# Kernel tuning notes

Measured on AMD Instinct MI355X. Metric: run time of the kernel, lower is better.

## Reference

```python
import jax, jax.numpy as jnp
import numpy as np

B, S, D, H = 1, 4096, 1024, 16
DH = D // H

def setup_inputs() -> dict:
    key = jax.random.key(0)
    ks = jax.random.split(key, 5)
    std = float(np.sqrt(2.0 / (D + D)))
    return {
        "x": jax.random.normal(ks[0], (B, S, D), dtype=jnp.float32),
        "Wq": jax.random.normal(ks[1], (D, D), dtype=jnp.float32) * std,
        "Wk": jax.random.normal(ks[2], (D, D), dtype=jnp.float32) * std,
        "Wv": jax.random.normal(ks[3], (D, D), dtype=jnp.float32) * std,
        "Wo": jax.random.normal(ks[4], (D, D), dtype=jnp.float32) * std,
    }

def reference(x, Wq, Wk, Wv, Wo):
    # projections: input @ W.T, then split heads: b s (h d) -> b h s d
    def split_heads(t):
        b, s, _ = t.shape
        return t.reshape(b, s, H, DH).transpose(0, 2, 1, 3)
    q = split_heads(x @ Wq.T)
    k = split_heads(x @ Wk.T)
    v = split_heads(x @ Wv.T)
    scale = 1.0 / jnp.sqrt(jnp.asarray(DH, dtype=x.dtype))
    scores = jnp.einsum("bhqd,bhkd->bhqk", q, k) * scale  # (b,h,s,s)
    # causal mask: allow k <= q
    causal = jnp.tril(jnp.ones((S, S), dtype=bool))
    scores = jnp.where(causal, scores, jnp.finfo(scores.dtype).min)
    attn = jax.nn.softmax(scores, axis=-1)
    out = jnp.einsum("bhqk,bhkd->bhqd", attn, v)  # (b,h,s,d)
    out = out.transpose(0, 2, 1, 3).reshape(B, S, D)  # b h s d -> b s (h d)
    return out @ Wo.T
```

## Files before the change

### kernel.cpp

```cpp
#include <hip/hip_runtime.h>
#include <math.h>

#define SEQ 4096
#define DM  1024
#define NH  16
#define DH  64

typedef _Float16 h16;
typedef __attribute__((ext_vector_type(4))) _Float16 h16x4;
typedef __attribute__((ext_vector_type(8))) _Float16 h16x8;
typedef __attribute__((ext_vector_type(4))) float f32x4;

__device__ __forceinline__ void gload_lds16(const h16* g, h16* l) {
    __builtin_amdgcn_global_load_lds(
        (const __attribute__((address_space(1))) void*)g,
        (__attribute__((address_space(3))) void*)l, 16, 0, 0);
}

__global__ __launch_bounds__(256) void cvt_f32_f16(const float* __restrict__ in,
                                                   h16* __restrict__ out, int n4) {
    const int i = blockIdx.x * 256 + threadIdx.x;
    if (i < n4) {
        const float4 v = ((const float4*)in)[i];
        h16x4 o = { (h16)v.x, (h16)v.y, (h16)v.z, (h16)v.w };
        ((h16x4*)out)[i] = o;
    }
}

#define GT 32

__global__ __launch_bounds__(256) void gemm_qkv(const h16* __restrict__ xh,
                                                const h16* __restrict__ Wq,
                                                const h16* __restrict__ Wk,
                                                const h16* __restrict__ Wv,
                                                h16* __restrict__ Qh,
                                                h16* __restrict__ Kh,
                                                h16* __restrict__ Vth,
                                                float scl) {
    __shared__ h16 As[128 * GT];
    __shared__ h16 Bs[128 * GT];

    const int z    = blockIdx.z;
    const h16* B   = (z == 0) ? Wq : (z == 1) ? Wk : Wv;
    const int t    = threadIdx.x;
    const int lane = t & 63;
    const int w    = t >> 6;
    const int wm   = (w >> 1) * 64;
    const int wn   = (w & 1) * 64;
    const int l15  = lane & 15;
    const int lq   = lane >> 4;
    const int lq8  = lq * 8;
    const int m0   = blockIdx.y * 128;
    const int n0   = blockIdx.x * 128;
    const int K = DM, M = SEQ, N = DM;

    const int srow = w * 16 + (lane >> 2);
    const int scol = (lane & 3) * 8;
    const h16* pa0 = xh + (size_t)(m0 + srow) * K + scol;
    const h16* pa1 = xh + (size_t)(m0 + 64 + srow) * K + scol;
    const h16* pb0 = B  + (size_t)(n0 + srow) * K + scol;
    const h16* pb1 = B  + (size_t)(n0 + 64 + srow) * K + scol;
    h16* const la0 = &As[w * 512];
    h16* const la1 = &As[2048 + w * 512];
    h16* const lb0 = &Bs[w * 512];
    h16* const lb1 = &Bs[2048 + w * 512];

    f32x4 acc[4][4] = {};

    for (int k0 = 0; k0 < K; k0 += 32) {
        __syncthreads();
        gload_lds16(pa0 + k0, la0);
        gload_lds16(pa1 + k0, la1);
        gload_lds16(pb0 + k0, lb0);
        gload_lds16(pb1 + k0, lb1);
        __syncthreads();

        h16x8 af[4], bf[4];
        #pragma unroll
        for (int i = 0; i < 4; ++i)
            af[i] = *(const h16x8*)&As[(wm + i * 16 + l15) * GT + lq8];
        #pragma unroll
        for (int j = 0; j < 4; ++j)
            bf[j] = *(const h16x8*)&Bs[(wn + j * 16 + l15) * GT + lq8];
        #pragma unroll
        for (int i = 0; i < 4; ++i)
            #pragma unroll
            for (int j = 0; j < 4; ++j)
                acc[i][j] = __builtin_amdgcn_mfma_f32_16x16x32_f16(af[i], bf[j], acc[i][j], 0, 0, 0);
    }

    const int cr = wm + lq * 4;
    const int cc = wn + l15;
    if (z == 2) {
        #pragma unroll
        for (int i = 0; i < 4; ++i)
            #pragma unroll
            for (int j = 0; j < 4; ++j) {
                const int gm0 = m0 + cr + i * 16;
                const int gn  = n0 + cc + j * 16;
                h16x4 v = { (h16)acc[i][j][0], (h16)acc[i][j][1],
                            (h16)acc[i][j][2], (h16)acc[i][j][3] };
                *(h16x4*)(Vth + (size_t)gn * M + gm0) = v;
            }
    } else {
        h16* Og = (z == 0) ? Qh : Kh;
        const float e = (z == 0) ? scl : 1.0f;
        #pragma unroll
        for (int i = 0; i < 4; ++i)
            #pragma unroll
            for (int j = 0; j < 4; ++j)
                #pragma unroll
                for (int r = 0; r < 4; ++r) {
                    const int gm = m0 + cr + i * 16 + r;
                    const int gn = n0 + cc + j * 16;
                    Og[(size_t)gm * N + gn] = (h16)(acc[i][j][r] * e);
                }
    }
}

__global__ __launch_bounds__(256) void gemm_out(const h16* __restrict__ A,
                                                const h16* __restrict__ B,
                                                float* __restrict__ C) {
    __shared__ h16 As[128 * GT];
    __shared__ h16 Bs[128 * GT];

    const int t    = threadIdx.x;
    const int lane = t & 63;
    const int w    = t >> 6;
    const int wm   = (w >> 1) * 64;
    const int wn   = (w & 1) * 64;
    const int l15  = lane & 15;
    const int lq   = lane >> 4;
    const int lq8  = lq * 8;
    const int m0   = blockIdx.y * 128;
    const int n0   = blockIdx.x * 128;
    const int K = DM, N = DM;

    const int srow = w * 16 + (lane >> 2);
    const int scol = (lane & 3) * 8;
    const h16* pa0 = A + (size_t)(m0 + srow) * K + scol;
    const h16* pa1 = A + (size_t)(m0 + 64 + srow) * K + scol;
    const h16* pb0 = B + (size_t)(n0 + srow) * K + scol;
    const h16* pb1 = B + (size_t)(n0 + 64 + srow) * K + scol;
    h16* const la0 = &As[w * 512];
    h16* const la1 = &As[2048 + w * 512];
    h16* const lb0 = &Bs[w * 512];
    h16* const lb1 = &Bs[2048 + w * 512];

    f32x4 acc[4][4] = {};

    for (int k0 = 0; k0 < K; k0 += 32) {
        __syncthreads();
        gload_lds16(pa0 + k0, la0);
        gload_lds16(pa1 + k0, la1);
        gload_lds16(pb0 + k0, lb0);
        gload_lds16(pb1 + k0, lb1);
        __syncthreads();

        h16x8 af[4], bf[4];
        #pragma unroll
        for (int i = 0; i < 4; ++i)
            af[i] = *(const h16x8*)&As[(wm + i * 16 + l15) * GT + lq8];
        #pragma unroll
        for (int j = 0; j < 4; ++j)
            bf[j] = *(const h16x8*)&Bs[(wn + j * 16 + l15) * GT + lq8];
        #pragma unroll
        for (int i = 0; i < 4; ++i)
            #pragma unroll
            for (int j = 0; j < 4; ++j)
                acc[i][j] = __builtin_amdgcn_mfma_f32_16x16x32_f16(af[i], bf[j], acc[i][j], 0, 0, 0);
    }

    const int cr = wm + lq * 4;
    const int cc = wn + l15;
    #pragma unroll
    for (int i = 0; i < 4; ++i)
        #pragma unroll
        for (int j = 0; j < 4; ++j)
            #pragma unroll
            for (int r = 0; r < 4; ++r)
                C[(size_t)(m0 + cr + i * 16 + r) * N + n0 + cc + j * 16] = acc[i][j][r];
}

#define AST 80

__device__ __forceinline__ void tile_softmax(f32x4 s[4], float& m_st, float& l_st,
                                             f32x4 o[4], h16* ps_row, bool diag,
                                             int q_loc, int lq) {
    if (diag) {
        #pragma unroll
        for (int jj = 0; jj < 4; ++jj)
            #pragma unroll
            for (int r = 0; r < 4; ++r)
                if ((jj * 16 + lq * 4 + r) > q_loc) s[jj][r] = -1e30f;
    }
    float mx = m_st;
    #pragma unroll
    for (int jj = 0; jj < 4; ++jj)
        #pragma unroll
        for (int r = 0; r < 4; ++r)
            mx = fmaxf(mx, s[jj][r]);
    mx = fmaxf(mx, __shfl_xor(mx, 16, 64));
    mx = fmaxf(mx, __shfl_xor(mx, 32, 64));
    const float alpha = exp2f(m_st - mx);
    m_st = mx;
    float sum = 0.0f;
    #pragma unroll
    for (int jj = 0; jj < 4; ++jj) {
        const float p0 = exp2f(s[jj][0] - mx);
        const float p1 = exp2f(s[jj][1] - mx);
        const float p2 = exp2f(s[jj][2] - mx);
        const float p3 = exp2f(s[jj][3] - mx);
        sum += (p0 + p1) + (p2 + p3);
        h16x4 pk = { (h16)p0, (h16)p1, (h16)p2, (h16)p3 };
        *(h16x4*)(ps_row + jj * 16 + lq * 4) = pk;
    }
    sum += __shfl_xor(sum, 16, 64);
    sum += __shfl_xor(sum, 32, 64);
    l_st = l_st * alpha + sum;
    #pragma unroll
    for (int jj = 0; jj < 4; ++jj)
        #pragma unroll
        for (int r = 0; r < 4; ++r)
            o[jj][r] *= alpha;
}

__global__ __launch_bounds__(256, 3) void flash_attn_mfma(
        const h16* __restrict__ Qg, const h16* __restrict__ Kg,
        const h16* __restrict__ Vt, h16* __restrict__ Og) {
    __shared__ h16 Ks[64 * AST];
    __shared__ h16 Vs[64 * AST];
    __shared__ h16 Ps[2][64 * AST];

    const int qA   = blockIdx.x;
    const int qB   = 63 - qA;
    const int hh   = blockIdx.y;
    const int t    = threadIdx.x;
    const int lane = t & 63;
    const int w    = t >> 6;
    const int l15  = lane & 15;
    const int lq   = lane >> 4;
    const int lq8  = lq * 8;
    const int hc   = hh * DH;
    const int q_loc = w * 16 + l15;

    const int r1 = t >> 3;
    const int r2 = r1 + 32;
    const int c1 = (t & 7) * 8;

    {
        const int qa0 = qA * 64, qb0 = qB * 64;
        *(h16x8*)&Ks[r1 * AST + c1] = *(const h16x8*)(Qg + (size_t)(qa0 + r1) * DM + hc + c1);
        *(h16x8*)&Ks[r2 * AST + c1] = *(const h16x8*)(Qg + (size_t)(qa0 + r2) * DM + hc + c1);
        *(h16x8*)&Vs[r1 * AST + c1] = *(const h16x8*)(Qg + (size_t)(qb0 + r1) * DM + hc + c1);
        *(h16x8*)&Vs[r2 * AST + c1] = *(const h16x8*)(Qg + (size_t)(qb0 + r2) * DM + hc + c1);
    }
    h16x8 kv1 = *(const h16x8*)(Kg + (size_t)(r1) * DM + hc + c1);
    h16x8 kv2 = *(const h16x8*)(Kg + (size_t)(r2) * DM + hc + c1);
    h16x8 vv1 = *(const h16x8*)(Vt + (size_t)(hc + r1) * SEQ + c1);
    h16x8 vv2 = *(const h16x8*)(Vt + (size_t)(hc + r2) * SEQ + c1);

    __syncthreads();
    h16x8 qfA[2], qfB[2];
    qfA[0] = *(const h16x8*)&Ks[q_loc * AST + lq8];
    qfA[1] = *(const h16x8*)&Ks[q_loc * AST + 32 + lq8];
    qfB[0] = *(const h16x8*)&Vs[q_loc * AST + lq8];
    qfB[1] = *(const h16x8*)&Vs[q_loc * AST + 32 + lq8];

    float mA = -1e30f, lA = 0.0f, mB = -1e30f, lB = 0.0f;
    f32x4 oA[4] = {}, oB[4] = {};
    h16* const psA = &Ps[0][(size_t)q_loc * AST];
    h16* const psB = &Ps[1][(size_t)q_loc * AST];

    int kt = 0;
    for (; kt <= qA; ++kt) {
        __syncthreads();
        *(h16x8*)&Ks[r1 * AST + c1] = kv1;
        *(h16x8*)&Ks[r2 * AST + c1] = kv2;
        *(h16x8*)&Vs[r1 * AST + c1] = vv1;
        *(h16x8*)&Vs[r2 * AST + c1] = vv2;
        __syncthreads();
        {
            const int k0n = (kt + 1) * 64;
            kv1 = *(const h16x8*)(Kg + (size_t)(k0n + r1) * DM + hc + c1);
            kv2 = *(const h16x8*)(Kg + (size_t)(k0n + r2) * DM + hc + c1);
            vv1 = *(const h16x8*)(Vt + (size_t)(hc + r1) * SEQ + k0n + c1);
            vv2 = *(const h16x8*)(Vt + (size_t)(hc + r2) * SEQ + k0n + c1);
        }

        f32x4 sA[4] = {}, sB[4] = {};
        #pragma unroll
        for (int kc = 0; kc < 2; ++kc)
            #pragma unroll
            for (int jj = 0; jj < 4; ++jj) {
                const h16x8 kf = *(const h16x8*)&Ks[(jj * 16 + l15) * AST + kc * 32 + lq8];
                sA[jj] = __builtin_amdgcn_mfma_f32_16x16x32_f16(kf, qfA[kc], sA[jj], 0, 0, 0);
                sB[jj] = __builtin_amdgcn_mfma_f32_16x16x32_f16(kf, qfB[kc], sB[jj], 0, 0, 0);
            }

        tile_softmax(sA, mA, lA, oA, psA, kt == qA, q_loc, lq);
        tile_softmax(sB, mB, lB, oB, psB, false, q_loc, lq);

        asm volatile("s_waitcnt lgkmcnt(0)" ::: "memory");
        h16x8 pfA[2], pfB[2];
        pfA[0] = *(const h16x8*)(psA + lq8);
        pfA[1] = *(const h16x8*)(psA + 32 + lq8);
        pfB[0] = *(const h16x8*)(psB + lq8);
        pfB[1] = *(const h16x8*)(psB + 32 + lq8);

        #pragma unroll
        for (int kc = 0; kc < 2; ++kc)
            #pragma unroll
            for (int jj = 0; jj < 4; ++jj) {
                const h16x8 vf = *(const h16x8*)&Vs[(jj * 16 + l15) * AST + kc * 32 + lq8];
                oA[jj] = __builtin_amdgcn_mfma_f32_16x16x32_f16(vf, pfA[kc], oA[jj], 0, 0, 0);
                oB[jj] = __builtin_amdgcn_mfma_f32_16x16x32_f16(vf, pfB[kc], oB[jj], 0, 0, 0);
            }
    }
    for (; kt <= qB; ++kt) {
        __syncthreads();
        *(h16x8*)&Ks[r1 * AST + c1] = kv1;
        *(h16x8*)&Ks[r2 * AST + c1] = kv2;
        *(h16x8*)&Vs[r1 * AST + c1] = vv1;
        *(h16x8*)&Vs[r2 * AST + c1] = vv2;
        __syncthreads();
        if (kt < qB) {
            const int k0n = (kt + 1) * 64;
            kv1 = *(const h16x8*)(Kg + (size_t)(k0n + r1) * DM + hc + c1);
            kv2 = *(const h16x8*)(Kg + (size_t)(k0n + r2) * DM + hc + c1);
            vv1 = *(const h16x8*)(Vt + (size_t)(hc + r1) * SEQ + k0n + c1);
            vv2 = *(const h16x8*)(Vt + (size_t)(hc + r2) * SEQ + k0n + c1);
        }

        f32x4 sB[4] = {};
        #pragma unroll
        for (int kc = 0; kc < 2; ++kc)
            #pragma unroll
            for (int jj = 0; jj < 4; ++jj) {
                const h16x8 kf = *(const h16x8*)&Ks[(jj * 16 + l15) * AST + kc * 32 + lq8];
                sB[jj] = __builtin_amdgcn_mfma_f32_16x16x32_f16(kf, qfB[kc], sB[jj], 0, 0, 0);
            }

        tile_softmax(sB, mB, lB, oB, psB, kt == qB, q_loc, lq);

        asm volatile("s_waitcnt lgkmcnt(0)" ::: "memory");
        h16x8 pfB[2];
        pfB[0] = *(const h16x8*)(psB + lq8);
        pfB[1] = *(const h16x8*)(psB + 32 + lq8);

        #pragma unroll
        for (int kc = 0; kc < 2; ++kc)
            #pragma unroll
            for (int jj = 0; jj < 4; ++jj) {
                const h16x8 vf = *(const h16x8*)&Vs[(jj * 16 + l15) * AST + kc * 32 + lq8];
                oB[jj] = __builtin_amdgcn_mfma_f32_16x16x32_f16(vf, pfB[kc], oB[jj], 0, 0, 0);
            }
    }

    {
        const float il = 1.0f / lA;
        const size_t qg = (size_t)(qA * 64 + q_loc) * DM + hc;
        #pragma unroll
        for (int jj = 0; jj < 4; ++jj) {
            h16x4 ov = { (h16)(oA[jj][0] * il), (h16)(oA[jj][1] * il),
                         (h16)(oA[jj][2] * il), (h16)(oA[jj][3] * il) };
            *(h16x4*)(Og + qg + jj * 16 + lq * 4) = ov;
        }
    }
    {
        const float il = 1.0f / lB;
        const size_t qg = (size_t)(qB * 64 + q_loc) * DM + hc;
        #pragma unroll
        for (int jj = 0; jj < 4; ++jj) {
            h16x4 ov = { (h16)(oB[jj][0] * il), (h16)(oB[jj][1] * il),
                         (h16)(oB[jj][2] * il), (h16)(oB[jj][3] * il) };
            *(h16x4*)(Og + qg + jj * 16 + lq * 4) = ov;
        }
    }
}

extern "C" void kernel_launch(void* const* d_in, const int* in_sizes, int n_in,
                              void* d_out, int out_size, void* d_ws, size_t ws_size,
                              hipStream_t stream) {
    const float* x  = (const float*)d_in[0];
    const float* Wq = (const float*)d_in[1];
    const float* Wk = (const float*)d_in[2];
    const float* Wv = (const float*)d_in[3];
    const float* Wo = (const float*)d_in[4];
    float* out = (float*)d_out;

    const size_t SD = (size_t)SEQ * DM;
    const size_t DD = (size_t)DM * DM;

    h16* xh  = (h16*)d_ws;
    h16* wqh = xh + SD;
    h16* wkh = wqh + DD;
    h16* wvh = wkh + DD;
    h16* woh = wvh + DD;
    h16* Qh  = woh + DD;
    h16* Kh  = Qh + SD;
    h16* Vth = Kh + SD;
    h16* AOh = Vth + SD;

    cvt_f32_f16<<<(int)(SD / 4 / 256), 256, 0, stream>>>(x,  xh,  (int)(SD / 4));
    cvt_f32_f16<<<(int)(DD / 4 / 256), 256, 0, stream>>>(Wq, wqh, (int)(DD / 4));
    cvt_f32_f16<<<(int)(DD / 4 / 256), 256, 0, stream>>>(Wk, wkh, (int)(DD / 4));
    cvt_f32_f16<<<(int)(DD / 4 / 256), 256, 0, stream>>>(Wv, wvh, (int)(DD / 4));
    cvt_f32_f16<<<(int)(DD / 4 / 256), 256, 0, stream>>>(Wo, woh, (int)(DD / 4));

    const dim3 blk(256);

    const float SCL = 0.125f * 1.44269504088896340736f;

    gemm_qkv<<<dim3(DM / 128, SEQ / 128, 3), blk, 0, stream>>>(
        xh, wqh, wkh, wvh, Qh, Kh, Vth, SCL);

    flash_attn_mfma<<<dim3(32, NH), blk, 0, stream>>>(Qh, Kh, Vth, AOh);

    gemm_out<<<dim3(DM / 128, SEQ / 128), blk, 0, stream>>>(AOh, woh, out);
}
```

Measured before the change: 237.2 us.

## Split paired-tile flash attention into one tile per block, fuse converts, widen GEMM K step

```diff
diff --git a/kernel.cpp b/kernel.cpp
--- a/kernel.cpp
+++ b/kernel.cpp
@@ -17,14 +17,27 @@
         (__attribute__((address_space(3))) void*)l, 16, 0, 0);
 }
 
-__global__ __launch_bounds__(256) void cvt_f32_f16(const float* __restrict__ in,
-                                                   h16* __restrict__ out, int n4) {
-    const int i = blockIdx.x * 256 + threadIdx.x;
-    if (i < n4) {
-        const float4 v = ((const float4*)in)[i];
-        h16x4 o = { (h16)v.x, (h16)v.y, (h16)v.z, (h16)v.w };
-        ((h16x4*)out)[i] = o;
-    }
+__global__ __launch_bounds__(256) void cvt_all(const float* __restrict__ x,
+                                               const float* __restrict__ wq,
+                                               const float* __restrict__ wk,
+                                               const float* __restrict__ wv,
+                                               const float* __restrict__ wo,
+                                               h16* __restrict__ dst) {
+    const size_t SD4 = (size_t)SEQ * DM / 4;
+    const size_t DD4 = (size_t)DM * DM / 4;
+    const size_t i = (size_t)blockIdx.x * 256 + threadIdx.x;
+    const float* src;
+    size_t off;
+    if (i < SD4) { src = x; off = i; }
+    else {
+        const size_t j = i - SD4;
+        const int wsel = (int)(j >> 18);
+        off = j & (DD4 - 1);
+        src = (wsel == 0) ? wq : (wsel == 1) ? wk : (wsel == 2) ? wv : wo;
+    }
+    const float4 v = ((const float4*)src)[off];
+    h16x4 o = { (h16)v.x, (h16)v.y, (h16)v.z, (h16)v.w };
+    ((h16x4*)dst)[i] = o;
 }
 
 #define GT 32
@@ -37,8 +50,8 @@
                                                 h16* __restrict__ Kh,
                                                 h16* __restrict__ Vth,
                                                 float scl) {
-    __shared__ h16 As[128 * GT];
-    __shared__ h16 Bs[128 * GT];
+    __shared__ h16 As[2][128 * GT];
+    __shared__ h16 Bs[2][128 * GT];
 
     const int z    = blockIdx.z;
     const h16* B   = (z == 0) ? Wq : (z == 1) ? Wk : Wv;
@@ -60,33 +73,36 @@
     const h16* pa1 = xh + (size_t)(m0 + 64 + srow) * K + scol;
     const h16* pb0 = B  + (size_t)(n0 + srow) * K + scol;
     const h16* pb1 = B  + (size_t)(n0 + 64 + srow) * K + scol;
-    h16* const la0 = &As[w * 512];
-    h16* const la1 = &As[2048 + w * 512];
-    h16* const lb0 = &Bs[w * 512];
-    h16* const lb1 = &Bs[2048 + w * 512];
 
     f32x4 acc[4][4] = {};
 
-    for (int k0 = 0; k0 < K; k0 += 32) {
-        __syncthreads();
-        gload_lds16(pa0 + k0, la0);
-        gload_lds16(pa1 + k0, la1);
-        gload_lds16(pb0 + k0, lb0);
-        gload_lds16(pb1 + k0, lb1);
-        __syncthreads();
-
-        h16x8 af[4], bf[4];
-        #pragma unroll
-        for (int i = 0; i < 4; ++i)
-            af[i] = *(const h16x8*)&As[(wm + i * 16 + l15) * GT + lq8];
-        #pragma unroll
-        for (int j = 0; j < 4; ++j)
-            bf[j] = *(const h16x8*)&Bs[(wn + j * 16 + l15) * GT + lq8];
-        #pragma unroll
-        for (int i = 0; i < 4; ++i)
+    for (int k0 = 0; k0 < K; k0 += 64) {
+        __syncthreads();
+        #pragma unroll
+        for (int s = 0; s < 2; ++s) {
+            const int ko = k0 + s * 32;
+            gload_lds16(pa0 + ko, &As[s][w * 512]);
+            gload_lds16(pa1 + ko, &As[s][2048 + w * 512]);
+            gload_lds16(pb0 + ko, &Bs[s][w * 512]);
+            gload_lds16(pb1 + ko, &Bs[s][2048 + w * 512]);
+        }
+        __syncthreads();
+
+        #pragma unroll
+        for (int s = 0; s < 2; ++s) {
+            h16x8 af[4], bf[4];
+            #pragma unroll
+            for (int i = 0; i < 4; ++i)
+                af[i] = *(const h16x8*)&As[s][(wm + i * 16 + l15) * GT + lq8];
             #pragma unroll
             for (int j = 0; j < 4; ++j)
-                acc[i][j] = __builtin_amdgcn_mfma_f32_16x16x32_f16(af[i], bf[j], acc[i][j], 0, 0, 0);
+                bf[j] = *(const h16x8*)&Bs[s][(wn + j * 16 + l15) * GT + lq8];
+            #pragma unroll
+            for (int i = 0; i < 4; ++i)
+                #pragma unroll
+                for (int j = 0; j < 4; ++j)
+                    acc[i][j] = __builtin_amdgcn_mfma_f32_16x16x32_f16(af[i], bf[j], acc[i][j], 0, 0, 0);
+        }
     }
 
     const int cr = wm + lq * 4;
@@ -121,8 +137,8 @@
 __global__ __launch_bounds__(256) void gemm_out(const h16* __restrict__ A,
                                                 const h16* __restrict__ B,
                                                 float* __restrict__ C) {
-    __shared__ h16 As[128 * GT];
-    __shared__ h16 Bs[128 * GT];
+    __shared__ h16 As[2][128 * GT];
+    __shared__ h16 Bs[2][128 * GT];
 
     const int t    = threadIdx.x;
     const int lane = t & 63;
@@ -142,33 +158,36 @@
     const h16* pa1 = A + (size_t)(m0 + 64 + srow) * K + scol;
     const h16* pb0 = B + (size_t)(n0 + srow) * K + scol;
     const h16* pb1 = B + (size_t)(n0 + 64 + srow) * K + scol;
-    h16* const la0 = &As[w * 512];
-    h16* const la1 = &As[2048 + w * 512];
-    h16* const lb0 = &Bs[w * 512];
-    h16* const lb1 = &Bs[2048 + w * 512];
 
     f32x4 acc[4][4] = {};
 
-    for (int k0 = 0; k0 < K; k0 += 32) {
-        __syncthreads();
-        gload_lds16(pa0 + k0, la0);
-        gload_lds16(pa1 + k0, la1);
-        gload_lds16(pb0 + k0, lb0);
-        gload_lds16(pb1 + k0, lb1);
-        __syncthreads();
-
-        h16x8 af[4], bf[4];
-        #pragma unroll
-        for (int i = 0; i < 4; ++i)
-            af[i] = *(const h16x8*)&As[(wm + i * 16 + l15) * GT + lq8];
-        #pragma unroll
-        for (int j = 0; j < 4; ++j)
-            bf[j] = *(const h16x8*)&Bs[(wn + j * 16 + l15) * GT + lq8];
-        #pragma unroll
-        for (int i = 0; i < 4; ++i)
+    for (int k0 = 0; k0 < K; k0 += 64) {
+        __syncthreads();
+        #pragma unroll
+        for (int s = 0; s < 2; ++s) {
+            const int ko = k0 + s * 32;
+            gload_lds16(pa0 + ko, &As[s][w * 512]);
+            gload_lds16(pa1 + ko, &As[s][2048 + w * 512]);
+            gload_lds16(pb0 + ko, &Bs[s][w * 512]);
+            gload_lds16(pb1 + ko, &Bs[s][2048 + w * 512]);
+        }
+        __syncthreads();
+
+        #pragma unroll
+        for (int s = 0; s < 2; ++s) {
+            h16x8 af[4], bf[4];
+            #pragma unroll
+            for (int i = 0; i < 4; ++i)
+                af[i] = *(const h16x8*)&As[s][(wm + i * 16 + l15) * GT + lq8];
             #pragma unroll
             for (int j = 0; j < 4; ++j)
-                acc[i][j] = __builtin_amdgcn_mfma_f32_16x16x32_f16(af[i], bf[j], acc[i][j], 0, 0, 0);
+                bf[j] = *(const h16x8*)&Bs[s][(wn + j * 16 + l15) * GT + lq8];
+            #pragma unroll
+            for (int i = 0; i < 4; ++i)
+                #pragma unroll
+                for (int j = 0; j < 4; ++j)
+                    acc[i][j] = __builtin_amdgcn_mfma_f32_16x16x32_f16(af[i], bf[j], acc[i][j], 0, 0, 0);
+        }
     }
 
     const int cr = wm + lq * 4;
@@ -183,58 +202,16 @@
 }
 
 #define AST 80
-
-__device__ __forceinline__ void tile_softmax(f32x4 s[4], float& m_st, float& l_st,
-                                             f32x4 o[4], h16* ps_row, bool diag,
-                                             int q_loc, int lq) {
-    if (diag) {
-        #pragma unroll
-        for (int jj = 0; jj < 4; ++jj)
-            #pragma unroll
-            for (int r = 0; r < 4; ++r)
-                if ((jj * 16 + lq * 4 + r) > q_loc) s[jj][r] = -1e30f;
-    }
-    float mx = m_st;
-    #pragma unroll
-    for (int jj = 0; jj < 4; ++jj)
-        #pragma unroll
-        for (int r = 0; r < 4; ++r)
-            mx = fmaxf(mx, s[jj][r]);
-    mx = fmaxf(mx, __shfl_xor(mx, 16, 64));
-    mx = fmaxf(mx, __shfl_xor(mx, 32, 64));
-    const float alpha = exp2f(m_st - mx);
-    m_st = mx;
-    float sum = 0.0f;
-    #pragma unroll
-    for (int jj = 0; jj < 4; ++jj) {
-        const float p0 = exp2f(s[jj][0] - mx);
-        const float p1 = exp2f(s[jj][1] - mx);
-        const float p2 = exp2f(s[jj][2] - mx);
-        const float p3 = exp2f(s[jj][3] - mx);
-        sum += (p0 + p1) + (p2 + p3);
-        h16x4 pk = { (h16)p0, (h16)p1, (h16)p2, (h16)p3 };
-        *(h16x4*)(ps_row + jj * 16 + lq * 4) = pk;
-    }
-    sum += __shfl_xor(sum, 16, 64);
-    sum += __shfl_xor(sum, 32, 64);
-    l_st = l_st * alpha + sum;
-    #pragma unroll
-    for (int jj = 0; jj < 4; ++jj)
-        #pragma unroll
-        for (int r = 0; r < 4; ++r)
-            o[jj][r] *= alpha;
-}
 
 __global__ __launch_bounds__(256, 3) void flash_attn_mfma(
         const h16* __restrict__ Qg, const h16* __restrict__ Kg,
         const h16* __restrict__ Vt, h16* __restrict__ Og) {
     __shared__ h16 Ks[64 * AST];
     __shared__ h16 Vs[64 * AST];
-    __shared__ h16 Ps[2][64 * AST];
-
-    const int qA   = blockIdx.x;
-    const int qB   = 63 - qA;
-    const int hh   = blockIdx.y;
+    __shared__ h16 Ps[64 * AST];
+
+    const int qt   = 63 - (int)blockIdx.y;
+    const int hh   = blockIdx.x;
     const int t    = threadIdx.x;
     const int lane = t & 63;
     const int w    = t >> 6;
@@ -242,45 +219,38 @@
     const int lq   = lane >> 4;
     const int lq8  = lq * 8;
     const int hc   = hh * DH;
+    const int q0   = qt * 64;
     const int q_loc = w * 16 + l15;
 
     const int r1 = t >> 3;
     const int r2 = r1 + 32;
     const int c1 = (t & 7) * 8;
 
-    {
-        const int qa0 = qA * 64, qb0 = qB * 64;
-        *(h16x8*)&Ks[r1 * AST + c1] = *(const h16x8*)(Qg + (size_t)(qa0 + r1) * DM + hc + c1);
-        *(h16x8*)&Ks[r2 * AST + c1] = *(const h16x8*)(Qg + (size_t)(qa0 + r2) * DM + hc + c1);
-        *(h16x8*)&Vs[r1 * AST + c1] = *(const h16x8*)(Qg + (size_t)(qb0 + r1) * DM + hc + c1);
-        *(h16x8*)&Vs[r2 * AST + c1] = *(const h16x8*)(Qg + (size_t)(qb0 + r2) * DM + hc + c1);
-    }
+    *(h16x8*)&Ks[r1 * AST + c1] = *(const h16x8*)(Qg + (size_t)(q0 + r1) * DM + hc + c1);
+    *(h16x8*)&Ks[r2 * AST + c1] = *(const h16x8*)(Qg + (size_t)(q0 + r2) * DM + hc + c1);
+
     h16x8 kv1 = *(const h16x8*)(Kg + (size_t)(r1) * DM + hc + c1);
     h16x8 kv2 = *(const h16x8*)(Kg + (size_t)(r2) * DM + hc + c1);
     h16x8 vv1 = *(const h16x8*)(Vt + (size_t)(hc + r1) * SEQ + c1);
     h16x8 vv2 = *(const h16x8*)(Vt + (size_t)(hc + r2) * SEQ + c1);
 
     __syncthreads();
-    h16x8 qfA[2], qfB[2];
-    qfA[0] = *(const h16x8*)&Ks[q_loc * AST + lq8];
-    qfA[1] = *(const h16x8*)&Ks[q_loc * AST + 32 + lq8];
-    qfB[0] = *(const h16x8*)&Vs[q_loc * AST + lq8];
-    qfB[1] = *(const h16x8*)&Vs[q_loc * AST + 32 + lq8];
-
-    float mA = -1e30f, lA = 0.0f, mB = -1e30f, lB = 0.0f;
-    f32x4 oA[4] = {}, oB[4] = {};
-    h16* const psA = &Ps[0][(size_t)q_loc * AST];
-    h16* const psB = &Ps[1][(size_t)q_loc * AST];
-
-    int kt = 0;
-    for (; kt <= qA; ++kt) {
+    h16x8 qf[2];
+    qf[0] = *(const h16x8*)&Ks[q_loc * AST + lq8];
+    qf[1] = *(const h16x8*)&Ks[q_loc * AST + 32 + lq8];
+
+    float m_st = -1e30f, l_st = 0.0f;
+    f32x4 o[4] = {};
+    h16* const ps = &Ps[(size_t)q_loc * AST];
+
+    for (int kt = 0; kt <= qt; ++kt) {
         __syncthreads();
         *(h16x8*)&Ks[r1 * AST + c1] = kv1;
         *(h16x8*)&Ks[r2 * AST + c1] = kv2;
         *(h16x8*)&Vs[r1 * AST + c1] = vv1;
         *(h16x8*)&Vs[r2 * AST + c1] = vv2;
         __syncthreads();
-        {
+        if (kt < qt) {
             const int k0n = (kt + 1) * 64;
             kv1 = *(const h16x8*)(Kg + (size_t)(k0n + r1) * DM + hc + c1);
             kv2 = *(const h16x8*)(Kg + (size_t)(k0n + r2) * DM + hc + c1);
@@ -288,94 +258,73 @@
             vv2 = *(const h16x8*)(Vt + (size_t)(hc + r2) * SEQ + k0n + c1);
         }
 
-        f32x4 sA[4] = {}, sB[4] = {};
+        f32x4 s[4] = {};
         #pragma unroll
         for (int kc = 0; kc < 2; ++kc)
             #pragma unroll
             for (int jj = 0; jj < 4; ++jj) {
                 const h16x8 kf = *(const h16x8*)&Ks[(jj * 16 + l15) * AST + kc * 32 + lq8];
-                sA[jj] = __builtin_amdgcn_mfma_f32_16x16x32_f16(kf, qfA[kc], sA[jj], 0, 0, 0);
-                sB[jj] = __builtin_amdgcn_mfma_f32_16x16x32_f16(kf, qfB[kc], sB[jj], 0, 0, 0);
+                s[jj] = __builtin_amdgcn_mfma_f32_16x16x32_f16(kf, qf[kc], s[jj], 0, 0, 0);
             }
 
-        tile_softmax(sA, mA, lA, oA, psA, kt == qA, q_loc, lq);
-        tile_softmax(sB, mB, lB, oB, psB, false, q_loc, lq);
+        if (kt == qt) {
+            #pragma unroll
+            for (int jj = 0; jj < 4; ++jj)
+                #pragma unroll
+                for (int r = 0; r < 4; ++r)
+                    if ((jj * 16 + lq * 4 + r) > q_loc) s[jj][r] = -1e30f;
+        }
+        float mx = m_st;
+        #pragma unroll
+        for (int jj = 0; jj < 4; ++jj)
+            #pragma unroll
+            for (int r = 0; r < 4; ++r)
+                mx = fmaxf(mx, s[jj][r]);
+        mx = fmaxf(mx, __shfl_xor(mx, 16, 64));
+        mx = fmaxf(mx, __shfl_xor(mx, 32, 64));
+        const float alpha = exp2f(m_st - mx);
+        m_st = mx;
+        float sum = 0.0f;
+        #pragma unroll
+        for (int jj = 0; jj < 4; ++jj) {
+            const float p0 = exp2f(s[jj][0] - mx);
+            const float p1 = exp2f(s[jj][1] - mx);
+            const float p2 = exp2f(s[jj][2] - mx);
+            const float p3 = exp2f(s[jj][3] - mx);
+            sum += (p0 + p1) + (p2 + p3);
+            h16x4 pk = { (h16)p0, (h16)p1, (h16)p2, (h16)p3 };
+            *(h16x4*)(ps + jj * 16 + lq * 4) = pk;
+        }
+        sum += __shfl_xor(sum, 16, 64);
+        sum += __shfl_xor(sum, 32, 64);
+        l_st = l_st * alpha + sum;
+        #pragma unroll
+        for (int jj = 0; jj < 4; ++jj)
+            #pragma unroll
+            for (int r = 0; r < 4; ++r)
+                o[jj][r] *= alpha;
 
         asm volatile("s_waitcnt lgkmcnt(0)" ::: "memory");
-        h16x8 pfA[2], pfB[2];
-        pfA[0] = *(const h16x8*)(psA + lq8);
-        pfA[1] = *(const h16x8*)(psA + 32 + lq8);
-        pfB[0] = *(const h16x8*)(psB + lq8);
-        pfB[1] = *(const h16x8*)(psB + 32 + lq8);
+        h16x8 pf[2];
+        pf[0] = *(const h16x8*)(ps + lq8);
+        pf[1] = *(const h16x8*)(ps + 32 + lq8);
 
         #pragma unroll
         for (int kc = 0; kc < 2; ++kc)
             #pragma unroll
             for (int jj = 0; jj < 4; ++jj) {
                 const h16x8 vf = *(const h16x8*)&Vs[(jj * 16 + l15) * AST + kc * 32 + lq8];
-                oA[jj] = __builtin_amdgcn_mfma_f32_16x16x32_f16(vf, pfA[kc], oA[jj], 0, 0, 0);
-                oB[jj] = __builtin_amdgcn_mfma_f32_16x16x32_f16(vf, pfB[kc], oB[jj], 0, 0, 0);
+                o[jj] = __builtin_amdgcn_mfma_f32_16x16x32_f16(vf, pf[kc], o[jj], 0, 0, 0);
             }
     }
-    for (; kt <= qB; ++kt) {
-        __syncthreads();
-        *(h16x8*)&Ks[r1 * AST + c1] = kv1;
-        *(h16x8*)&Ks[r2 * AST + c1] = kv2;
-        *(h16x8*)&Vs[r1 * AST + c1] = vv1;
-        *(h16x8*)&Vs[r2 * AST + c1] = vv2;
-        __syncthreads();
-        if (kt < qB) {
-            const int k0n = (kt + 1) * 64;
-            kv1 = *(const h16x8*)(Kg + (size_t)(k0n + r1) * DM + hc + c1);
-            kv2 = *(const h16x8*)(Kg + (size_t)(k0n + r2) * DM + hc + c1);
-            vv1 = *(const h16x8*)(Vt + (size_t)(hc + r1) * SEQ + k0n + c1);
-            vv2 = *(const h16x8*)(Vt + (size_t)(hc + r2) * SEQ + k0n + c1);
-        }
-
-        f32x4 sB[4] = {};
-        #pragma unroll
-        for (int kc = 0; kc < 2; ++kc)
-            #pragma unroll
-            for (int jj = 0; jj < 4; ++jj) {
-                const h16x8 kf = *(const h16x8*)&Ks[(jj * 16 + l15) * AST + kc * 32 + lq8];
-                sB[jj] = __builtin_amdgcn_mfma_f32_16x16x32_f16(kf, qfB[kc], sB[jj], 0, 0, 0);
-            }
-
-        tile_softmax(sB, mB, lB, oB, psB, kt == qB, q_loc, lq);
-
-        asm volatile("s_waitcnt lgkmcnt(0)" ::: "memory");
-        h16x8 pfB[2];
-        pfB[0] = *(const h16x8*)(psB + lq8);
-        pfB[1] = *(const h16x8*)(psB + 32 + lq8);
-
-        #pragma unroll
-        for (int kc = 0; kc < 2; ++kc)
-            #pragma unroll
-            for (int jj = 0; jj < 4; ++jj) {
-                const h16x8 vf = *(const h16x8*)&Vs[(jj * 16 + l15) * AST + kc * 32 + lq8];
-                oB[jj] = __builtin_amdgcn_mfma_f32_16x16x32_f16(vf, pfB[kc], oB[jj], 0, 0, 0);
-            }
-    }
-
-    {
-        const float il = 1.0f / lA;
-        const size_t qg = (size_t)(qA * 64 + q_loc) * DM + hc;
-        #pragma unroll
-        for (int jj = 0; jj < 4; ++jj) {
-            h16x4 ov = { (h16)(oA[jj][0] * il), (h16)(oA[jj][1] * il),
-                         (h16)(oA[jj][2] * il), (h16)(oA[jj][3] * il) };
-            *(h16x4*)(Og + qg + jj * 16 + lq * 4) = ov;
-        }
-    }
-    {
-        const float il = 1.0f / lB;
-        const size_t qg = (size_t)(qB * 64 + q_loc) * DM + hc;
-        #pragma unroll
-        for (int jj = 0; jj < 4; ++jj) {
-            h16x4 ov = { (h16)(oB[jj][0] * il), (h16)(oB[jj][1] * il),
-                         (h16)(oB[jj][2] * il), (h16)(oB[jj][3] * il) };
-            *(h16x4*)(Og + qg + jj * 16 + lq * 4) = ov;
-        }
+
+    const float il = 1.0f / l_st;
+    const size_t qg = (size_t)(q0 + q_loc) * DM + hc;
+    #pragma unroll
+    for (int jj = 0; jj < 4; ++jj) {
+        h16x4 ov = { (h16)(o[jj][0] * il), (h16)(o[jj][1] * il),
+                     (h16)(o[jj][2] * il), (h16)(o[jj][3] * il) };
+        *(h16x4*)(Og + qg + jj * 16 + lq * 4) = ov;
     }
 }
 
@@ -402,20 +351,16 @@
     h16* Vth = Kh + SD;
     h16* AOh = Vth + SD;
 
-    cvt_f32_f16<<<(int)(SD / 4 / 256), 256, 0, stream>>>(x,  xh,  (int)(SD / 4));
-    cvt_f32_f16<<<(int)(DD / 4 / 256), 256, 0, stream>>>(Wq, wqh, (int)(DD / 4));
-    cvt_f32_f16<<<(int)(DD / 4 / 256), 256, 0, stream>>>(Wk, wkh, (int)(DD / 4));
-    cvt_f32_f16<<<(int)(DD / 4 / 256), 256, 0, stream>>>(Wv, wvh, (int)(DD / 4));
-    cvt_f32_f16<<<(int)(DD / 4 / 256), 256, 0, stream>>>(Wo, woh, (int)(DD / 4));
-
     const dim3 blk(256);
+
+    cvt_all<<<(int)((SD + 4 * DD) / 4 / 256), blk, 0, stream>>>(x, Wq, Wk, Wv, Wo, xh);
 
     const float SCL = 0.125f * 1.44269504088896340736f;
 
     gemm_qkv<<<dim3(DM / 128, SEQ / 128, 3), blk, 0, stream>>>(
         xh, wqh, wkh, wvh, Qh, Kh, Vth, SCL);
 
-    flash_attn_mfma<<<dim3(32, NH), blk, 0, stream>>>(Qh, Kh, Vth, AOh);
+    flash_attn_mfma<<<dim3(NH, 64), blk, 0, stream>>>(Qh, Kh, Vth, AOh);
 
     gemm_out<<<dim3(DM / 128, SEQ / 128), blk, 0, stream>>>(AOh, woh, out);
 }
```

Measured after the change: 233.4 us. About the same (-1.6%).
